# Performance work log

Hardware: AMD Instinct MI355X
Metric: run time of the kernel (lower is better)

Reference implementation:

```python
import jax, jax.numpy as jnp
import numpy as np

N_NODES = 100000
N_EDGES = 1200000
N_FEAT = 128
HIDDEN = 64
N_GRAPHS = 256


def setup_inputs() -> dict:
    key = jax.random.key(0)
    ks = jax.random.split(key, 8)
    x = jax.random.normal(ks[0], (N_NODES, N_FEAT), dtype=jnp.float32)
    edge_index = jax.random.randint(ks[1], (2, N_EDGES), 0, N_NODES, dtype=jnp.int64)
    batch = jnp.sort(jax.random.randint(ks[2], (N_NODES,), 0, N_GRAPHS, dtype=jnp.int64))
    W1 = jax.random.normal(ks[3], (N_FEAT, HIDDEN), dtype=jnp.float32) * (1.0 / np.sqrt(N_FEAT))
    b1 = jnp.zeros((HIDDEN,), dtype=jnp.float32)
    W2 = jax.random.normal(ks[4], (HIDDEN, HIDDEN), dtype=jnp.float32) * (1.0 / np.sqrt(HIDDEN))
    b2 = jnp.zeros((HIDDEN,), dtype=jnp.float32)
    Wl = jax.random.normal(ks[5], (HIDDEN, 1), dtype=jnp.float32) * (1.0 / np.sqrt(HIDDEN))
    bl = jnp.zeros((1,), dtype=jnp.float32)
    return {"x": x, "edge_index": edge_index, "batch": batch,
            "W1": W1, "b1": b1, "W2": W2, "b2": b2, "Wl": Wl, "bl": bl}


def _gcn_conv(x, src, dst, W, b, n):
    # PyG GCNConv: linear transform, then sym-normalized scatter-add (self-loops already in src/dst)
    h = x @ W  # [N, out]
    deg = jax.ops.segment_sum(jnp.ones(src.shape[0], x.dtype), dst, num_segments=n)
    dinv = jnp.where(deg > 0, jax.lax.rsqrt(deg), jnp.zeros_like(deg))
    norm = dinv[src] * dinv[dst]  # [E+N]
    out = jax.ops.segment_sum(norm[:, None] * h[src], dst, num_segments=n)
    return out + b


def reference(x, edge_index, batch, W1, b1, W2, b2, Wl, bl):
    n = x.shape[0]
    loops = jnp.arange(n, dtype=edge_index.dtype)
    src = jnp.concatenate([edge_index[0], loops])
    dst = jnp.concatenate([edge_index[1], loops])
    h = _gcn_conv(x, src, dst, W1, b1, n)
    h = jax.nn.relu(h)
    h = _gcn_conv(h, src, dst, W2, b2, n)
    # global mean pool over graphs
    sums = jax.ops.segment_sum(h, batch, num_segments=N_GRAPHS)
    cnts = jax.ops.segment_sum(jnp.ones((n,), h.dtype), batch, num_segments=N_GRAPHS)
    pooled = sums / jnp.maximum(cnts, 1.0)[:, None]
    return pooled @ Wl + bl
```

## Files before the change

### kernel.cpp

```cpp
#include <hip/hip_runtime.h>

#define N_NODES 100000
#define N_EDGES 1200000
#define R_BUCKETS 256
#define RSZ 400
#define CAP 8192
#define CH 4096
#define NC 293

typedef _Float16 h8 __attribute__((ext_vector_type(8)));
typedef _Float16 h2 __attribute__((ext_vector_type(2)));
typedef float f32x16 __attribute__((ext_vector_type(16)));

__global__ __launch_bounds__(256) void bkt_scatter(const int* __restrict__ src,
                                                   const int* __restrict__ dst,
                                                   int* __restrict__ bucket_alloc,
                                                   int* __restrict__ ebuf, int E) {
    __shared__ int h[R_BUCKETS];
    __shared__ int off[R_BUCKETS];
    h[threadIdx.x] = 0;
    __syncthreads();
    int e0 = blockIdx.x * CH;
    int e1 = min(e0 + CH, E);
    for (int e = e0 + (int)threadIdx.x; e < e1; e += 256)
        atomicAdd(&h[dst[e] / RSZ], 1);
    __syncthreads();
    int b = threadIdx.x;
    int hc = h[b];
    off[b] = b * CAP + (hc > 0 ? atomicAdd(&bucket_alloc[b], hc) : 0);
    __syncthreads();
    for (int e = e0 + (int)threadIdx.x; e < e1; e += 256) {
        int d = dst[e];
        int bk = d / RSZ;
        int p = atomicAdd(&off[bk], 1);
        ebuf[p] = (src[e] << 9) | (d - bk * RSZ);
    }
}

__global__ __launch_bounds__(256) void bkt_build(const int* __restrict__ ebuf,
                                                 const int* __restrict__ bcnt,
                                                 int2* __restrict__ row2,
                                                 float* __restrict__ dinv,
                                                 int* __restrict__ csr, int N) {
    __shared__ int hist[RSZ];
    __shared__ int pref[RSZ];
    __shared__ int part[256];
    int r = blockIdx.x;
    int nbase = r * RSZ;
    int ebase = r * CAP;
    int ecnt = bcnt[r];
    for (int i = threadIdx.x; i < RSZ; i += 256) hist[i] = 0;
    __syncthreads();
    for (int e = (int)threadIdx.x; e < ecnt; e += 256)
        atomicAdd(&hist[ebuf[ebase + e] & 511], 1);
    __syncthreads();
    for (int i = threadIdx.x; i < RSZ; i += 256) {
        int gi = nbase + i;
        if (gi < N) dinv[gi] = rsqrtf((float)hist[i] + 1.0f);
    }
    int s0 = threadIdx.x * 2;
    int sum = (s0 < RSZ) ? hist[s0] + hist[s0 + 1] : 0;
    part[threadIdx.x] = sum;
    __syncthreads();
    for (int off = 1; off < 256; off <<= 1) {
        int v = (threadIdx.x >= off) ? part[threadIdx.x - off] : 0;
        __syncthreads();
        part[threadIdx.x] += v;
        __syncthreads();
    }
    if (s0 < RSZ) {
        int run = part[threadIdx.x] - sum;
        pref[s0] = run;
        pref[s0 + 1] = run + hist[s0];
    }
    __syncthreads();
    for (int i = threadIdx.x; i < RSZ; i += 256) {
        int gi = nbase + i;
        if (gi < N) row2[gi] = make_int2(ebase + pref[i], ebase + pref[i] + hist[i]);
    }
    __syncthreads();
    for (int e = (int)threadIdx.x; e < ecnt; e += 256) {
        int epk = ebuf[ebase + e];
        int t = atomicAdd(&pref[epk & 511], 1);
        csr[ebase + t] = (int)(((unsigned)epk) >> 9);
    }
}

__global__ void prep_kernel(const float* __restrict__ W1, const float* __restrict__ W2,
                            const float* __restrict__ Wl, float* __restrict__ w2l,
                            _Float16* __restrict__ whi, _Float16* __restrict__ wlo) {
    if (blockIdx.x == 32) {
        if (threadIdx.x < 64) {
            int f = threadIdx.x;
            float s = 0.0f;
            for (int o = 0; o < 64; o++) s += W2[f * 64 + o] * Wl[o];
            w2l[f] = s;
        }
        return;
    }
    int idx = blockIdx.x * 256 + threadIdx.x;
    int j = idx & 7;
    int lane = (idx >> 3) & 63;
    int kk = (idx >> 9) & 7;
    int nt = idx >> 12;
    int k = kk * 16 + (lane >> 5) * 8 + j;
    int n = nt * 32 + (lane & 31);
    float v = W1[k * 64 + n];
    _Float16 hi = (_Float16)v;
    whi[idx] = hi;
    wlo[idx] = (_Float16)(v - (float)hi);
}

__global__ __launch_bounds__(256) void gemm_mfma(const float* __restrict__ x,
                                                 const _Float16* __restrict__ whi,
                                                 const _Float16* __restrict__ wlo,
                                                 const float* __restrict__ dinv,
                                                 _Float16* __restrict__ out, int N) {
    int wave = threadIdx.x >> 6;
    int lane = threadIdx.x & 63;
    int base = blockIdx.x * 128 + wave * 32;
    int row = base + (lane & 31);
    int rowc = min(row, N - 1);
    const float* xrow = x + (size_t)rowc * 128 + (lane >> 5) * 8;

    f32x16 acc0, acc1;
#pragma unroll
    for (int i = 0; i < 16; i++) { acc0[i] = 0.f; acc1[i] = 0.f; }

#pragma unroll
    for (int kk = 0; kk < 8; kk++) {
        float4 xa = *reinterpret_cast<const float4*>(xrow + kk * 16);
        float4 xb = *reinterpret_cast<const float4*>(xrow + kk * 16 + 4);
        float xv[8] = {xa.x, xa.y, xa.z, xa.w, xb.x, xb.y, xb.z, xb.w};
        h8 ahi, alo;
#pragma unroll
        for (int j = 0; j < 8; j++) {
            _Float16 hi = (_Float16)xv[j];
            ahi[j] = hi;
            alo[j] = (_Float16)(xv[j] - (float)hi);
        }
        h8 b0h = *reinterpret_cast<const h8*>(whi + (size_t)(kk * 64 + lane) * 8);
        h8 b0l = *reinterpret_cast<const h8*>(wlo + (size_t)(kk * 64 + lane) * 8);
        h8 b1h = *reinterpret_cast<const h8*>(whi + (size_t)((8 + kk) * 64 + lane) * 8);
        h8 b1l = *reinterpret_cast<const h8*>(wlo + (size_t)((8 + kk) * 64 + lane) * 8);
        acc0 = __builtin_amdgcn_mfma_f32_32x32x16_f16(ahi, b0h, acc0, 0, 0, 0);
        acc0 = __builtin_amdgcn_mfma_f32_32x32x16_f16(ahi, b0l, acc0, 0, 0, 0);
        acc0 = __builtin_amdgcn_mfma_f32_32x32x16_f16(alo, b0h, acc0, 0, 0, 0);
        acc1 = __builtin_amdgcn_mfma_f32_32x32x16_f16(ahi, b1h, acc1, 0, 0, 0);
        acc1 = __builtin_amdgcn_mfma_f32_32x32x16_f16(ahi, b1l, acc1, 0, 0, 0);
        acc1 = __builtin_amdgcn_mfma_f32_32x32x16_f16(alo, b1h, acc1, 0, 0, 0);
    }

    int col = lane & 31;
    int rbase = base + 4 * (lane >> 5);
#pragma unroll
    for (int reg = 0; reg < 16; reg++) {
        int node = rbase + (reg & 3) + 8 * (reg >> 2);
        if (node < N) {
            float di = dinv[node];
            out[(size_t)node * 64 + col] = (_Float16)(di * acc0[reg]);
            out[(size_t)node * 64 + 32 + col] = (_Float16)(di * acc1[reg]);
        }
    }
}

#define AGG_NPB 32
__global__ __launch_bounds__(256) void agg1_kernel(const _Float16* __restrict__ t,
                                                   const int2* __restrict__ row2,
                                                   const int* __restrict__ csr,
                                                   const float* __restrict__ dinv,
                                                   const float* __restrict__ b1,
                                                   const float* __restrict__ w2l,
                                                   float* __restrict__ q, int N) {
    int lane = threadIdx.x & 63;
    int w = threadIdx.x >> 6;
    int hl = lane & 31;
    int hsel = lane >> 5;
    float2 b1v = reinterpret_cast<const float2*>(b1)[hl];
    float2 wlv = reinterpret_cast<const float2*>(w2l)[hl];
    int i0 = blockIdx.x * AGG_NPB;
    int iend = min(i0 + AGG_NPB, N);
    for (int ip = i0 + 2 * w; ip < iend; ip += 8) {
        int iA = ip;
        int iB = ip + 1;
        bool hasB = iB < iend;
        int2 rrA = row2[iA];
        int2 rrB = hasB ? row2[iB] : make_int2(rrA.x, rrA.x);
        int myi = hsel ? iB : iA;
        int myic = min(myi, N - 1);
        int rs = hsel ? rrB.x : rrA.x;
        int re = hsel ? rrB.y : rrA.y;
        int deg = re - rs;
        int kmax = max(rrA.y - rrA.x, rrB.y - rrB.x);
        int rlast = max(re - 1, rs);
        h2 sv = *reinterpret_cast<const h2*>(t + ((size_t)myic << 6) + (hl << 1));
        float a0 = (float)sv[0];
        float a1 = (float)sv[1];
        for (int base = 0; base < kmax; base += 32) {
            int sp = min(csr[min(rs + base + hl, rlast)] & 0x1FFFF, N - 1);
            int kend = min(kmax - base, 32);
            for (int k = 0; k < kend; k += 8) {
                h2 vv[8];
#pragma unroll
                for (int j = 0; j < 8; j++) {
                    int s = __shfl(sp, k + j, 32);
                    vv[j] = *reinterpret_cast<const h2*>(t + ((size_t)s << 6) + (hl << 1));
                }
#pragma unroll
                for (int j = 0; j < 8; j++) {
                    if (base + k + j < deg) {
                        a0 += (float)vv[j][0];
                        a1 += (float)vv[j][1];
                    }
                }
            }
        }
        float di = dinv[myic];
        float h0 = fmaxf(di * a0 + b1v.x, 0.f);
        float h1 = fmaxf(di * a1 + b1v.y, 0.f);
        float p = h0 * wlv.x + h1 * wlv.y;
        p += __shfl_xor(p, 1, 64);
        p += __shfl_xor(p, 2, 64);
        p += __shfl_xor(p, 4, 64);
        p += __shfl_xor(p, 8, 64);
        p += __shfl_xor(p, 16, 64);
        if (hl == 0 && myi < iend) q[myi] = di * p;
    }
}

__global__ __launch_bounds__(256) void agg2_pool_kernel(const float* __restrict__ q,
                                                        const int2* __restrict__ row2,
                                                        const int* __restrict__ csr,
                                                        const float* __restrict__ dinv,
                                                        const int* __restrict__ batch,
                                                        float* __restrict__ gsum, int N) {
    __shared__ float bins[256];
    bins[threadIdx.x] = 0.0f;
    __syncthreads();
    int i = blockIdx.x * 256 + threadIdx.x;
    if (i < N) {
        int2 rr = row2[i];
        float acc = q[i];
        for (int j = rr.x; j < rr.y; j++) acc += q[csr[j]];
        atomicAdd(&bins[batch[i]], dinv[i] * acc);
    }
    __syncthreads();
    int i0 = blockIdx.x * 256;
    if (i0 < N) {
        int ilast = min(i0 + 255, N - 1);
        int gmin = batch[i0];
        int gmax = batch[ilast];
        for (int g = gmin + (int)threadIdx.x; g <= gmax; g += 256)
            atomicAdd(&gsum[g], bins[g]);
    }
}

__global__ void out_kernel(const float* __restrict__ gsum, const int* __restrict__ batch,
                           const float* __restrict__ b2, const float* __restrict__ Wl,
                           const float* __restrict__ bl, float* __restrict__ out, int N) {
    int g = threadIdx.x;
    int lo = 0, hi = N;
    while (lo < hi) { int m = (lo + hi) >> 1; if (batch[m] < g) lo = m + 1; else hi = m; }
    int start = lo;
    hi = N;
    while (lo < hi) { int m = (lo + hi) >> 1; if (batch[m] < g + 1) lo = m + 1; else hi = m; }
    int cnt = lo - start;
    float c = 0.0f;
    for (int f = 0; f < 64; f++) c += b2[f] * Wl[f];
    out[g] = gsum[g] / fmaxf((float)cnt, 1.0f) + c + bl[0];
}

extern "C" void kernel_launch(void* const* d_in, const int* in_sizes, int n_in,
                              void* d_out, int out_size, void* d_ws, size_t ws_size,
                              hipStream_t stream) {
    const float* x  = (const float*)d_in[0];
    const int*   ei = (const int*)d_in[1];
    const int*   batch = (const int*)d_in[2];
    const float* W1 = (const float*)d_in[3];
    const float* b1 = (const float*)d_in[4];
    const float* W2 = (const float*)d_in[5];
    const float* b2 = (const float*)d_in[6];
    const float* Wl = (const float*)d_in[7];
    const float* bl = (const float*)d_in[8];
    float* out = (float*)d_out;

    const int N = N_NODES, E = N_EDGES;
    const int nblk = (N + 255) / 256;
    const int* src = ei;
    const int* dst = ei + E;

    char* ws = (char*)d_ws;
    int*      ebuf      = (int*)ws;       ws += (size_t)R_BUCKETS * CAP * 4;
    int*      csr       = (int*)ws;       ws += (size_t)R_BUCKETS * CAP * 4;
    _Float16* buf1      = (_Float16*)ws;  ws += 6400000 * 2;
    int2*     row2      = (int2*)ws;      ws += 100096 * 8;
    float*    dinv      = (float*)ws;     ws += 100096 * 4;
    float*    q         = (float*)ws;     ws += 100096 * 4;
    float*    gsum      = (float*)ws;     ws += 256 * 4;
    int*      bucket_alloc = (int*)ws;    ws += 256 * 4;
    float*    w2l       = (float*)ws;     ws += 256 * 4;
    _Float16* whi       = (_Float16*)ws;  ws += 8192 * 2;
    _Float16* wlo       = (_Float16*)ws;  ws += 8192 * 2;

    hipMemsetAsync(gsum, 0, 2048, stream);

    bkt_scatter<<<NC, 256, 0, stream>>>(src, dst, bucket_alloc, ebuf, E);
    bkt_build<<<R_BUCKETS, 256, 0, stream>>>(ebuf, bucket_alloc, row2, dinv, csr, N);

    prep_kernel<<<33, 256, 0, stream>>>(W1, W2, Wl, w2l, whi, wlo);

    gemm_mfma<<<(N + 127) / 128, 256, 0, stream>>>(x, whi, wlo, dinv, buf1, N);

    agg1_kernel<<<(N + AGG_NPB - 1) / AGG_NPB, 256, 0, stream>>>(
        buf1, row2, csr, dinv, b1, w2l, q, N);

    agg2_pool_kernel<<<nblk, 256, 0, stream>>>(q, row2, csr, dinv, batch, gsum, N);

    out_kernel<<<1, 256, 0, stream>>>(gsum, batch, b2, Wl, bl, out, N);
}
```

Measured before the change: 208.8 us.

## Drop CSR build; aggregate directly from dst buckets with LDS atomics

Removes the per-bucket CSR build kernel. Degrees are now counted with global atomics during scatter, and weight prep is folded into the scatter kernel. Both aggregation layers consume the unsorted bucketed edge list and accumulate into shared-memory rows with atomics, and a last-block pattern fuses the final pooling output kernel into agg2. This trades the sort/CSR pass and several launches for heavy LDS float atomics, plus global degree atomics that may contend.

```diff
diff --git a/kernel.cpp b/kernel.cpp
--- a/kernel.cpp
+++ b/kernel.cpp
@@ -7,88 +7,47 @@
 #define CAP 8192
 #define CH 4096
 #define NC 293
+#define APAD 65
 
 typedef _Float16 h8 __attribute__((ext_vector_type(8)));
 typedef _Float16 h2 __attribute__((ext_vector_type(2)));
 typedef float f32x16 __attribute__((ext_vector_type(16)));
 
-__global__ __launch_bounds__(256) void bkt_scatter(const int* __restrict__ src,
-                                                   const int* __restrict__ dst,
-                                                   int* __restrict__ bucket_alloc,
-                                                   int* __restrict__ ebuf, int E) {
+__global__ __launch_bounds__(256) void scatter_deg_prep(const int* __restrict__ src,
+                                                        const int* __restrict__ dst,
+                                                        int* __restrict__ bucket_alloc,
+                                                        int* __restrict__ ebuf,
+                                                        int* __restrict__ deg,
+                                                        const float* __restrict__ W1,
+                                                        const float* __restrict__ W2,
+                                                        const float* __restrict__ Wl,
+                                                        float* __restrict__ w2l,
+                                                        _Float16* __restrict__ whi,
+                                                        _Float16* __restrict__ wlo, int E) {
     __shared__ int h[R_BUCKETS];
     __shared__ int off[R_BUCKETS];
+    __shared__ int dcache[CH];
     h[threadIdx.x] = 0;
     __syncthreads();
     int e0 = blockIdx.x * CH;
     int e1 = min(e0 + CH, E);
-    for (int e = e0 + (int)threadIdx.x; e < e1; e += 256)
-        atomicAdd(&h[dst[e] / RSZ], 1);
+    for (int e = e0 + (int)threadIdx.x; e < e1; e += 256) {
+        int d = dst[e];
+        dcache[e - e0] = d;
+        atomicAdd(&h[d / RSZ], 1);
+        atomicAdd(&deg[d], 1);
+    }
     __syncthreads();
     int b = threadIdx.x;
     int hc = h[b];
     off[b] = b * CAP + (hc > 0 ? atomicAdd(&bucket_alloc[b], hc) : 0);
     __syncthreads();
     for (int e = e0 + (int)threadIdx.x; e < e1; e += 256) {
-        int d = dst[e];
+        int d = dcache[e - e0];
         int bk = d / RSZ;
         int p = atomicAdd(&off[bk], 1);
         ebuf[p] = (src[e] << 9) | (d - bk * RSZ);
     }
-}
-
-__global__ __launch_bounds__(256) void bkt_build(const int* __restrict__ ebuf,
-                                                 const int* __restrict__ bcnt,
-                                                 int2* __restrict__ row2,
-                                                 float* __restrict__ dinv,
-                                                 int* __restrict__ csr, int N) {
-    __shared__ int hist[RSZ];
-    __shared__ int pref[RSZ];
-    __shared__ int part[256];
-    int r = blockIdx.x;
-    int nbase = r * RSZ;
-    int ebase = r * CAP;
-    int ecnt = bcnt[r];
-    for (int i = threadIdx.x; i < RSZ; i += 256) hist[i] = 0;
-    __syncthreads();
-    for (int e = (int)threadIdx.x; e < ecnt; e += 256)
-        atomicAdd(&hist[ebuf[ebase + e] & 511], 1);
-    __syncthreads();
-    for (int i = threadIdx.x; i < RSZ; i += 256) {
-        int gi = nbase + i;
-        if (gi < N) dinv[gi] = rsqrtf((float)hist[i] + 1.0f);
-    }
-    int s0 = threadIdx.x * 2;
-    int sum = (s0 < RSZ) ? hist[s0] + hist[s0 + 1] : 0;
-    part[threadIdx.x] = sum;
-    __syncthreads();
-    for (int off = 1; off < 256; off <<= 1) {
-        int v = (threadIdx.x >= off) ? part[threadIdx.x - off] : 0;
-        __syncthreads();
-        part[threadIdx.x] += v;
-        __syncthreads();
-    }
-    if (s0 < RSZ) {
-        int run = part[threadIdx.x] - sum;
-        pref[s0] = run;
-        pref[s0 + 1] = run + hist[s0];
-    }
-    __syncthreads();
-    for (int i = threadIdx.x; i < RSZ; i += 256) {
-        int gi = nbase + i;
-        if (gi < N) row2[gi] = make_int2(ebase + pref[i], ebase + pref[i] + hist[i]);
-    }
-    __syncthreads();
-    for (int e = (int)threadIdx.x; e < ecnt; e += 256) {
-        int epk = ebuf[ebase + e];
-        int t = atomicAdd(&pref[epk & 511], 1);
-        csr[ebase + t] = (int)(((unsigned)epk) >> 9);
-    }
-}
-
-__global__ void prep_kernel(const float* __restrict__ W1, const float* __restrict__ W2,
-                            const float* __restrict__ Wl, float* __restrict__ w2l,
-                            _Float16* __restrict__ whi, _Float16* __restrict__ wlo) {
     if (blockIdx.x == 32) {
         if (threadIdx.x < 64) {
             int f = threadIdx.x;
@@ -96,25 +55,25 @@
             for (int o = 0; o < 64; o++) s += W2[f * 64 + o] * Wl[o];
             w2l[f] = s;
         }
-        return;
-    }
-    int idx = blockIdx.x * 256 + threadIdx.x;
-    int j = idx & 7;
-    int lane = (idx >> 3) & 63;
-    int kk = (idx >> 9) & 7;
-    int nt = idx >> 12;
-    int k = kk * 16 + (lane >> 5) * 8 + j;
-    int n = nt * 32 + (lane & 31);
-    float v = W1[k * 64 + n];
-    _Float16 hi = (_Float16)v;
-    whi[idx] = hi;
-    wlo[idx] = (_Float16)(v - (float)hi);
+    } else if (blockIdx.x < 32) {
+        int idx = blockIdx.x * 256 + threadIdx.x;
+        int j = idx & 7;
+        int lane = (idx >> 3) & 63;
+        int kk = (idx >> 9) & 7;
+        int nt = idx >> 12;
+        int k = kk * 16 + (lane >> 5) * 8 + j;
+        int n = nt * 32 + (lane & 31);
+        float v = W1[k * 64 + n];
+        _Float16 hi = (_Float16)v;
+        whi[idx] = hi;
+        wlo[idx] = (_Float16)(v - (float)hi);
+    }
 }
 
 __global__ __launch_bounds__(256) void gemm_mfma(const float* __restrict__ x,
                                                  const _Float16* __restrict__ whi,
                                                  const _Float16* __restrict__ wlo,
-                                                 const float* __restrict__ dinv,
+                                                 const int* __restrict__ deg,
                                                  _Float16* __restrict__ out, int N) {
     int wave = threadIdx.x >> 6;
     int lane = threadIdx.x & 63;
@@ -157,65 +116,73 @@
     for (int reg = 0; reg < 16; reg++) {
         int node = rbase + (reg & 3) + 8 * (reg >> 2);
         if (node < N) {
-            float di = dinv[node];
+            float di = rsqrtf((float)deg[node] + 1.0f);
             out[(size_t)node * 64 + col] = (_Float16)(di * acc0[reg]);
             out[(size_t)node * 64 + 32 + col] = (_Float16)(di * acc1[reg]);
         }
     }
 }
 
-#define AGG_NPB 32
-__global__ __launch_bounds__(256) void agg1_kernel(const _Float16* __restrict__ t,
-                                                   const int2* __restrict__ row2,
-                                                   const int* __restrict__ csr,
-                                                   const float* __restrict__ dinv,
-                                                   const float* __restrict__ b1,
-                                                   const float* __restrict__ w2l,
-                                                   float* __restrict__ q, int N) {
-    int lane = threadIdx.x & 63;
-    int w = threadIdx.x >> 6;
+__global__ __launch_bounds__(1024) void agg1_bucket(const _Float16* __restrict__ t,
+                                                    const int* __restrict__ ebuf,
+                                                    const int* __restrict__ bcnt,
+                                                    const int* __restrict__ deg,
+                                                    const float* __restrict__ b1,
+                                                    const float* __restrict__ w2l,
+                                                    float* __restrict__ q, int N) {
+    extern __shared__ float acc[];
+    int tid = (int)threadIdx.x;
+    int lane = tid & 63;
+    int wid = tid >> 6;
     int hl = lane & 31;
     int hsel = lane >> 5;
+    int r = blockIdx.x;
+    int nbase = r * RSZ;
+    int ebase = r * CAP;
+    int ecnt = bcnt[r];
+    for (int i = tid; i < RSZ * APAD; i += 1024) acc[i] = 0.f;
+    __syncthreads();
+
+    for (int eb = wid * 64; eb < ecnt; eb += 1024) {
+        int rec = 0;
+        if (eb + lane < ecnt) rec = ebuf[ebase + eb + lane];
+#pragma unroll
+        for (int kb = 0; kb < 32; kb += 16) {
+            h2 vv[16];
+            int dl[16];
+#pragma unroll
+            for (int k = 0; k < 16; k++) {
+                int j = 2 * (kb + k) + hsel;
+                int rj = __shfl(rec, j, 64);
+                dl[k] = rj;
+                int s = rj >> 9;
+                vv[k] = *reinterpret_cast<const h2*>(t + ((size_t)s << 6) + (hl << 1));
+            }
+#pragma unroll
+            for (int k = 0; k < 16; k++) {
+                int j = 2 * (kb + k) + hsel;
+                if (eb + j < ecnt) {
+                    int dloc = dl[k] & 511;
+                    atomicAdd(&acc[dloc * APAD + 2 * hl], (float)vv[k][0]);
+                    atomicAdd(&acc[dloc * APAD + 2 * hl + 1], (float)vv[k][1]);
+                }
+            }
+        }
+    }
+    __syncthreads();
+
+    int halfid = (wid << 1) | hsel;
     float2 b1v = reinterpret_cast<const float2*>(b1)[hl];
     float2 wlv = reinterpret_cast<const float2*>(w2l)[hl];
-    int i0 = blockIdx.x * AGG_NPB;
-    int iend = min(i0 + AGG_NPB, N);
-    for (int ip = i0 + 2 * w; ip < iend; ip += 8) {
-        int iA = ip;
-        int iB = ip + 1;
-        bool hasB = iB < iend;
-        int2 rrA = row2[iA];
-        int2 rrB = hasB ? row2[iB] : make_int2(rrA.x, rrA.x);
-        int myi = hsel ? iB : iA;
-        int myic = min(myi, N - 1);
-        int rs = hsel ? rrB.x : rrA.x;
-        int re = hsel ? rrB.y : rrA.y;
-        int deg = re - rs;
-        int kmax = max(rrA.y - rrA.x, rrB.y - rrB.x);
-        int rlast = max(re - 1, rs);
-        h2 sv = *reinterpret_cast<const h2*>(t + ((size_t)myic << 6) + (hl << 1));
-        float a0 = (float)sv[0];
-        float a1 = (float)sv[1];
-        for (int base = 0; base < kmax; base += 32) {
-            int sp = min(csr[min(rs + base + hl, rlast)] & 0x1FFFF, N - 1);
-            int kend = min(kmax - base, 32);
-            for (int k = 0; k < kend; k += 8) {
-                h2 vv[8];
-#pragma unroll
-                for (int j = 0; j < 8; j++) {
-                    int s = __shfl(sp, k + j, 32);
-                    vv[j] = *reinterpret_cast<const h2*>(t + ((size_t)s << 6) + (hl << 1));
-                }
-#pragma unroll
-                for (int j = 0; j < 8; j++) {
-                    if (base + k + j < deg) {
-                        a0 += (float)vv[j][0];
-                        a1 += (float)vv[j][1];
-                    }
-                }
-            }
-        }
-        float di = dinv[myic];
+    for (int iloc = halfid; iloc < RSZ; iloc += 32) {
+        int i = nbase + iloc;
+        if (i >= N) break;
+        float a0 = acc[iloc * APAD + 2 * hl];
+        float a1 = acc[iloc * APAD + 2 * hl + 1];
+        h2 sv = *reinterpret_cast<const h2*>(t + ((size_t)i << 6) + (hl << 1));
+        a0 += (float)sv[0];
+        a1 += (float)sv[1];
+        float di = rsqrtf((float)deg[i] + 1.0f);
         float h0 = fmaxf(di * a0 + b1v.x, 0.f);
         float h1 = fmaxf(di * a1 + b1v.y, 0.f);
         float p = h0 * wlv.x + h1 * wlv.y;
@@ -224,50 +191,89 @@
         p += __shfl_xor(p, 4, 64);
         p += __shfl_xor(p, 8, 64);
         p += __shfl_xor(p, 16, 64);
-        if (hl == 0 && myi < iend) q[myi] = di * p;
-    }
-}
-
-__global__ __launch_bounds__(256) void agg2_pool_kernel(const float* __restrict__ q,
-                                                        const int2* __restrict__ row2,
-                                                        const int* __restrict__ csr,
-                                                        const float* __restrict__ dinv,
-                                                        const int* __restrict__ batch,
-                                                        float* __restrict__ gsum, int N) {
+        if (hl == 0) q[i] = di * p;
+    }
+}
+
+__global__ __launch_bounds__(1024) void agg2_bucket(const float* __restrict__ q,
+                                                    const int* __restrict__ ebuf,
+                                                    const int* __restrict__ bcnt,
+                                                    const int* __restrict__ deg,
+                                                    const int* __restrict__ batch,
+                                                    float* __restrict__ gsum,
+                                                    float* __restrict__ gcnt,
+                                                    int* __restrict__ done,
+                                                    const float* __restrict__ b2,
+                                                    const float* __restrict__ Wl,
+                                                    const float* __restrict__ bl,
+                                                    float* __restrict__ out, int N) {
+    __shared__ float qacc[RSZ];
     __shared__ float bins[256];
-    bins[threadIdx.x] = 0.0f;
-    __syncthreads();
-    int i = blockIdx.x * 256 + threadIdx.x;
-    if (i < N) {
-        int2 rr = row2[i];
-        float acc = q[i];
-        for (int j = rr.x; j < rr.y; j++) acc += q[csr[j]];
-        atomicAdd(&bins[batch[i]], dinv[i] * acc);
-    }
-    __syncthreads();
-    int i0 = blockIdx.x * 256;
-    if (i0 < N) {
-        int ilast = min(i0 + 255, N - 1);
-        int gmin = batch[i0];
+    __shared__ float cbins[256];
+    __shared__ int lastflag;
+    int tid = (int)threadIdx.x;
+    int r = blockIdx.x;
+    int nbase = r * RSZ;
+    int ebase = r * CAP;
+    int ecnt = bcnt[r];
+    if (tid < RSZ) qacc[tid] = 0.f;
+    if (tid < 256) { bins[tid] = 0.f; cbins[tid] = 0.f; }
+    __syncthreads();
+
+    int e0 = 0;
+    for (; e0 + 4096 <= ecnt; e0 += 4096) {
+        int r0 = ebuf[ebase + e0 + tid];
+        int r1 = ebuf[ebase + e0 + tid + 1024];
+        int r2 = ebuf[ebase + e0 + tid + 2048];
+        int r3 = ebuf[ebase + e0 + tid + 3072];
+        float q0 = q[r0 >> 9];
+        float q1 = q[r1 >> 9];
+        float q2 = q[r2 >> 9];
+        float q3 = q[r3 >> 9];
+        atomicAdd(&qacc[r0 & 511], q0);
+        atomicAdd(&qacc[r1 & 511], q1);
+        atomicAdd(&qacc[r2 & 511], q2);
+        atomicAdd(&qacc[r3 & 511], q3);
+    }
+    for (int e = e0 + tid; e < ecnt; e += 1024) {
+        int rr = ebuf[ebase + e];
+        atomicAdd(&qacc[rr & 511], q[rr >> 9]);
+    }
+    __syncthreads();
+
+    if (tid < RSZ) {
+        int i = nbase + tid;
+        if (i < N) {
+            float di = rsqrtf((float)deg[i] + 1.0f);
+            float val = di * (q[i] + qacc[tid]);
+            int g = batch[i];
+            atomicAdd(&bins[g], val);
+            atomicAdd(&cbins[g], 1.0f);
+        }
+    }
+    __syncthreads();
+
+    if (nbase < N) {
+        int ilast = min(nbase + RSZ - 1, N - 1);
+        int gmin = batch[nbase];
         int gmax = batch[ilast];
-        for (int g = gmin + (int)threadIdx.x; g <= gmax; g += 256)
+        for (int g = gmin + tid; g <= gmax; g += 1024) {
             atomicAdd(&gsum[g], bins[g]);
-    }
-}
-
-__global__ void out_kernel(const float* __restrict__ gsum, const int* __restrict__ batch,
-                           const float* __restrict__ b2, const float* __restrict__ Wl,
-                           const float* __restrict__ bl, float* __restrict__ out, int N) {
-    int g = threadIdx.x;
-    int lo = 0, hi = N;
-    while (lo < hi) { int m = (lo + hi) >> 1; if (batch[m] < g) lo = m + 1; else hi = m; }
-    int start = lo;
-    hi = N;
-    while (lo < hi) { int m = (lo + hi) >> 1; if (batch[m] < g + 1) lo = m + 1; else hi = m; }
-    int cnt = lo - start;
-    float c = 0.0f;
-    for (int f = 0; f < 64; f++) c += b2[f] * Wl[f];
-    out[g] = gsum[g] / fmaxf((float)cnt, 1.0f) + c + bl[0];
+            atomicAdd(&gcnt[g], cbins[g]);
+        }
+    }
+    __threadfence();
+    __syncthreads();
+    if (tid == 0) lastflag = (atomicAdd(done, 1) == R_BUCKETS - 1) ? 1 : 0;
+    __syncthreads();
+    if (lastflag && tid < 256) {
+        int g = tid;
+        float s = atomicAdd(&gsum[g], 0.0f);
+        float c = atomicAdd(&gcnt[g], 0.0f);
+        float dot = 0.f;
+        for (int f = 0; f < 64; f++) dot += b2[f] * Wl[f];
+        out[g] = s / fmaxf(c, 1.0f) + dot + bl[0];
+    }
 }
 
 extern "C" void kernel_launch(void* const* d_in, const int* in_sizes, int n_in,
@@ -285,36 +291,32 @@
     float* out = (float*)d_out;
 
     const int N = N_NODES, E = N_EDGES;
-    const int nblk = (N + 255) / 256;
     const int* src = ei;
     const int* dst = ei + E;
 
     char* ws = (char*)d_ws;
     int*      ebuf      = (int*)ws;       ws += (size_t)R_BUCKETS * CAP * 4;
-    int*      csr       = (int*)ws;       ws += (size_t)R_BUCKETS * CAP * 4;
     _Float16* buf1      = (_Float16*)ws;  ws += 6400000 * 2;
-    int2*     row2      = (int2*)ws;      ws += 100096 * 8;
-    float*    dinv      = (float*)ws;     ws += 100096 * 4;
+    int*      deg       = (int*)ws;       ws += 100096 * 4;
+    float*    gsum      = (float*)ws;     ws += 256 * 4;
+    float*    gcnt      = (float*)ws;     ws += 256 * 4;
+    int*      bucket_alloc = (int*)ws;    ws += 256 * 4;
+    int*      done      = (int*)ws;       ws += 256 * 4;
     float*    q         = (float*)ws;     ws += 100096 * 4;
-    float*    gsum      = (float*)ws;     ws += 256 * 4;
-    int*      bucket_alloc = (int*)ws;    ws += 256 * 4;
     float*    w2l       = (float*)ws;     ws += 256 * 4;
     _Float16* whi       = (_Float16*)ws;  ws += 8192 * 2;
     _Float16* wlo       = (_Float16*)ws;  ws += 8192 * 2;
 
-    hipMemsetAsync(gsum, 0, 2048, stream);
-
-    bkt_scatter<<<NC, 256, 0, stream>>>(src, dst, bucket_alloc, ebuf, E);
-    bkt_build<<<R_BUCKETS, 256, 0, stream>>>(ebuf, bucket_alloc, row2, dinv, csr, N);
-
-    prep_kernel<<<33, 256, 0, stream>>>(W1, W2, Wl, w2l, whi, wlo);
-
-    gemm_mfma<<<(N + 127) / 128, 256, 0, stream>>>(x, whi, wlo, dinv, buf1, N);
-
-    agg1_kernel<<<(N + AGG_NPB - 1) / AGG_NPB, 256, 0, stream>>>(
-        buf1, row2, csr, dinv, b1, w2l, q, N);
-
-    agg2_pool_kernel<<<nblk, 256, 0, stream>>>(q, row2, csr, dinv, batch, gsum, N);
-
-    out_kernel<<<1, 256, 0, stream>>>(gsum, batch, b2, Wl, bl, out, N);
-}
+    hipMemsetAsync(deg, 0, 400384 + 4096, stream);
+
+    scatter_deg_prep<<<NC, 256, 0, stream>>>(src, dst, bucket_alloc, ebuf, deg,
+                                             W1, W2, Wl, w2l, whi, wlo, E);
+
+    gemm_mfma<<<(N + 127) / 128, 256, 0, stream>>>(x, whi, wlo, deg, buf1, N);
+
+    agg1_bucket<<<R_BUCKETS, 1024, RSZ * APAD * 4, stream>>>(
+        buf1, ebuf, bucket_alloc, deg, b1, w2l, q, N);
+
+    agg2_bucket<<<R_BUCKETS, 1024, 0, stream>>>(q, ebuf, bucket_alloc, deg, batch,
+                                                gsum, gcnt, done, b2, Wl, bl, out, N);
+}
```

Result: slower. 667.0 us (+219.4%).
